# Optimization experiments

Measured on AMD Instinct MI355X. Metric: run time of the kernel, lower is better.

Reference implementation:

```python
import jax, jax.numpy as jnp
import numpy as np

EPS = 1e-3  # keras LayerNormalization default epsilon


def _layernorm(x, gamma, beta):
    mu = jnp.mean(x, axis=-1, keepdims=True)
    var = jnp.mean(jnp.square(x - mu), axis=-1, keepdims=True)
    return (x - mu) * jax.lax.rsqrt(var + EPS) * gamma + beta


def setup_inputs() -> dict:
    key = jax.random.key(0)
    B, T, D, H = 8, 2048, 192, 3
    KD = D           # TalkingHeadsAttention(key_dim=dim, value_dim=dim)
    HID = 4 * D      # mlp_ratio = 4.0
    ks = jax.random.split(key, 12)
    s_in = 0.02
    inp = {
        "x": jax.random.normal(ks[0], (B, T, D), jnp.float32),
        # norm1 / norm2
        "gamma1": jnp.ones((D,), jnp.float32),
        "beta1": jnp.zeros((D,), jnp.float32),
        "gamma2": jnp.ones((D,), jnp.float32),
        "beta2": jnp.zeros((D,), jnp.float32),
        # attention projections (qkv_bias=False -> no biases)
        "wq": jax.random.normal(ks[1], (D, H, KD), jnp.float32) * s_in,
        "wk": jax.random.normal(ks[2], (D, H, KD), jnp.float32) * s_in,
        "wv": jax.random.normal(ks[3], (D, H, KD), jnp.float32) * s_in,
        "wo": jax.random.normal(ks[4], (H, KD, D), jnp.float32) * s_in,
        # talking-heads mixing matrices [H, H]
        "pre_w": jnp.eye(H, dtype=jnp.float32) + jax.random.normal(ks[5], (H, H), jnp.float32) * 0.02,
        "post_w": jnp.eye(H, dtype=jnp.float32) + jax.random.normal(ks[6], (H, H), jnp.float32) * 0.02,
        # MLP (bias=True)
        "w1": jax.random.normal(ks[7], (D, HID), jnp.float32) * s_in,
        "b1": jnp.zeros((HID,), jnp.float32),
        "w2": jax.random.normal(ks[8], (HID, D), jnp.float32) * s_in,
        "b2": jnp.zeros((D,), jnp.float32),
    }
    return inp


def reference(x, gamma1, beta1, gamma2, beta2, wq, wk, wv, wo, pre_w, post_w, w1, b1, w2, b2):
    KD = wq.shape[-1]
    # --- pre-norm + talking-heads attention ---
    n = _layernorm(x, gamma1, beta1)                      # [B,T,D]
    q = jnp.einsum("btd,dhk->bthk", n, wq)               # [B,T,H,KD]
    k = jnp.einsum("bsd,dhk->bshk", n, wk)
    v = jnp.einsum("bsd,dhk->bshk", n, wv)
    scores = jnp.einsum("bthk,bshk->bhts", q, k) / jnp.sqrt(jnp.asarray(KD, x.dtype))
    scores = jnp.einsum("bhts,hg->bgts", scores, pre_w)   # pre-softmax head mix
    probs = jax.nn.softmax(scores, axis=-1)
    probs = jnp.einsum("bhts,hg->bgts", probs, post_w)    # post-softmax head mix
    ctx = jnp.einsum("bhts,bshk->bthk", probs, v)         # [B,T,H,KD]
    attn_out = jnp.einsum("bthk,hkd->btd", ctx, wo)       # [B,T,D]
    x = x + attn_out                                      # ls1/drop_path1 are Identity
    # --- pre-norm + MLP ---
    n2 = _layernorm(x, gamma2, beta2)
    h = jax.nn.gelu(n2 @ w1 + b1, approximate=False)      # keras gelu = exact erf
    mlp_out = h @ w2 + b2
    return x + mlp_out
```

## Files before the change

kernel.cpp:

```cpp
#include <hip/hip_runtime.h>
#include <hip/hip_bf16.h>

typedef __hip_bfloat16 bf16;
typedef unsigned char u8;
typedef __attribute__((ext_vector_type(8))) __bf16 bf16x8;
typedef __attribute__((ext_vector_type(4))) float f32x4;
typedef __attribute__((ext_vector_type(2))) float f32x2;

__device__ __forceinline__ void gld_lds16(const void* g, void* l) {
  __builtin_amdgcn_global_load_lds((const __attribute__((address_space(1))) void*)g,
                                   (__attribute__((address_space(3))) void*)l, 16, 0, 0);
}
__device__ __forceinline__ u8 f2e4m3(float v) {
  return (u8)(__builtin_amdgcn_cvt_pk_fp8_f32(v, 0.f, 0, false) & 0xff);
}
__device__ __forceinline__ f32x2 pk_mul(f32x2 a, f32x2 b) {
  f32x2 d;
  asm("v_pk_mul_f32 %0, %1, %2" : "=v"(d) : "v"(a), "v"(b));
  return d;
}
__device__ __forceinline__ f32x2 pk_fma(f32x2 a, f32x2 b, f32x2 c) {
  f32x2 d;
  asm("v_pk_fma_f32 %0, %1, %2, %3" : "=v"(d) : "v"(a), "v"(b), "v"(c));
  return d;
}

__global__ __launch_bounds__(256) void setup_k(
    const float* __restrict__ x, const float* __restrict__ gamma1, const float* __restrict__ beta1,
    const float* __restrict__ wq, const float* __restrict__ wk,
    const float* __restrict__ wv, const float* __restrict__ wo,
    const float* __restrict__ post_w, const float* __restrict__ w1, const float* __restrict__ w2,
    bf16* __restrict__ nb, bf16* __restrict__ WqkvT,
    bf16* __restrict__ w1T, bf16* __restrict__ w2f)
{
  const int bid = blockIdx.x;
  if (bid < 432) {
    const int j = bid * 256 + threadIdx.x;
    const int dd = j % 192;
    const int r = j / 192;
    const int h = r / 192, din = r % 192;
    float acc = 0.f;
    #pragma unroll
    for (int g2 = 0; g2 < 3; ++g2) {
      const float pw = post_w[h*3 + g2];
      const float* wvp = wv + (size_t)din*576 + g2*192;
      const float* wop = wo + (size_t)(g2*192)*192 + dd;
      float s0 = 0.f, s1 = 0.f, s2 = 0.f, s3 = 0.f;
      for (int kd = 0; kd < 192; kd += 4) {
        s0 += wvp[kd]     * wop[(size_t)kd*192];
        s1 += wvp[kd + 1] * wop[(size_t)(kd + 1)*192];
        s2 += wvp[kd + 2] * wop[(size_t)(kd + 2)*192];
        s3 += wvp[kd + 3] * wop[(size_t)(kd + 3)*192];
      }
      acc += pw * ((s0 + s1) + (s2 + s3));
    }
    WqkvT[(size_t)(1152 + h*192 + dd)*192 + din] = __float2bfloat16(acc);
    return;
  }
  if (bid < 2448) {
    int i = (bid - 432) * 256 + threadIdx.x;
    if (i < 221184) {
      int n = i / 192, d = i % 192;
      int sel = n / 576, c = n % 576, h = c / 192, kd = c % 192;
      const float* w = (sel == 0) ? wq : wk;
      WqkvT[i] = __float2bfloat16(w[(d*3 + h)*192 + kd]);
      return;
    }
    i -= 221184;
    if (i < 147456) {
      int j = i / 192, d = i % 192;
      w1T[i] = __float2bfloat16(w1[d*768 + j]);
      return;
    }
    i -= 147456;
    {
      int j = i / 192, d = i % 192;
      int c = j >> 6, ks = (j >> 5) & 1, l4 = (j >> 3) & 3, e = j & 7;
      int dn = d >> 4, l15 = d & 15;
      w2f[(size_t)((((c*2 + ks)*12 + dn)*64) + l4*16 + l15)*8 + e] =
          __float2bfloat16(w2[(size_t)j*192 + d]);
    }
    return;
  }
  {
    int row = (bid - 2448) * 4 + (threadIdx.x >> 6);
    int lane = threadIdx.x & 63;
    const float* xr = x + (size_t)row * 192;
    float v0 = xr[lane], v1 = xr[lane + 64], v2 = xr[lane + 128];
    float s = v0 + v1 + v2;
    #pragma unroll
    for (int o = 32; o; o >>= 1) s += __shfl_xor(s, o);
    float mu = s * (1.f / 192.f);
    float d0 = v0 - mu, d1 = v1 - mu, d2 = v2 - mu;
    float q = d0*d0 + d1*d1 + d2*d2;
    #pragma unroll
    for (int o = 32; o; o >>= 1) q += __shfl_xor(q, o);
    float rs = rsqrtf(q * (1.f / 192.f) + 1e-3f);
    bf16* orow = nb + (size_t)row * 192;
    orow[lane]       = __float2bfloat16(d0*rs*gamma1[lane]       + beta1[lane]);
    orow[lane + 64]  = __float2bfloat16(d1*rs*gamma1[lane + 64]  + beta1[lane + 64]);
    orow[lane + 128] = __float2bfloat16(d2*rs*gamma1[lane + 128] + beta1[lane + 128]);
  }
}

__global__ __launch_bounds__(256) void gemm_qkv(
    const bf16* __restrict__ A, const bf16* __restrict__ BT,
    u8* __restrict__ q_out, u8* __restrict__ k_out, u8* __restrict__ mt_out)
{
  const int K = 192;
  const int tid = threadIdx.x, lane = tid & 63, wid = tid >> 6;
  const int wm = wid >> 1, wn = wid & 1;
  const int row0 = blockIdx.y * 128, col0 = blockIdx.x * 64;
  __shared__ __align__(16) bf16 As[2][128 * 32];
  __shared__ __align__(16) bf16 Bs[2][64 * 32];
  f32x4 acc[4][2] = {};

#define STAGE(buf_, kt_) do { \
    const bf16* Ab_ = A + (size_t)row0 * K + (kt_) * 32; \
    int c0_ = tid, r0_ = c0_ >> 2, cc0_ = (c0_ & 3) << 3; \
    gld_lds16(Ab_ + (size_t)r0_ * K + cc0_, &As[buf_][c0_ * 8]); \
    int c1_ = tid + 256, r1_ = c1_ >> 2, cc1_ = (c1_ & 3) << 3; \
    gld_lds16(Ab_ + (size_t)r1_ * K + cc1_, &As[buf_][c1_ * 8]); \
    const bf16* Bb_ = BT + (size_t)col0 * K + (kt_) * 32; \
    gld_lds16(Bb_ + (size_t)(tid >> 2) * K + ((tid & 3) << 3), &Bs[buf_][tid * 8]); \
  } while (0)

  STAGE(0, 0);
  for (int kt = 0; kt < 6; ++kt) {
    __syncthreads();
    const int buf = kt & 1;
    if (kt + 1 < 6) STAGE(buf ^ 1, kt + 1);
    const int koff = (lane >> 4) * 8;
    bf16x8 af[4], bfr[2];
    #pragma unroll
    for (int m = 0; m < 4; ++m)
      af[m] = *(const bf16x8*)&As[buf][(wm*64 + m*16 + (lane & 15))*32 + koff];
    #pragma unroll
    for (int n = 0; n < 2; ++n)
      bfr[n] = *(const bf16x8*)&Bs[buf][(wn*32 + n*16 + (lane & 15))*32 + koff];
    #pragma unroll
    for (int m = 0; m < 4; ++m)
      #pragma unroll
      for (int n = 0; n < 2; ++n)
        acc[m][n] = __builtin_amdgcn_mfma_f32_16x16x32_bf16(af[m], bfr[n], acc[m][n], 0, 0, 0);
  }
#undef STAGE

  const int rbase = row0 + wm * 64;
  const int cbase = col0 + wn * 32;
  #pragma unroll
  for (int m = 0; m < 4; ++m) {
    #pragma unroll
    for (int n = 0; n < 2; ++n) {
      const int col = cbase + n*16 + (lane & 15);
      const int rtop = rbase + m*16 + ((lane >> 4) << 2);
      const int b = rtop >> 11, t_ = rtop & 2047;
      const int sel = col / 576, c2 = col % 576;
      const int h = c2 / 192, kd = c2 % 192;
      if (sel == 2) {
        int pk = __builtin_amdgcn_cvt_pk_fp8_f32(acc[m][n][0], acc[m][n][1], 0, false);
        pk = __builtin_amdgcn_cvt_pk_fp8_f32(acc[m][n][2], acc[m][n][3], pk, true);
        const size_t fo = ((((size_t)b*64 + (t_>>5))*3 + h)*12 + (kd>>4))*512
                        + (((kd&15) + (((t_>>3)&3)<<4))<<3) + (t_&4);
        *(unsigned*)&mt_out[fo] = (unsigned)pk;
      } else {
        #pragma unroll
        for (int j = 0; j < 4; ++j) {
          const int t = t_ + j;
          const size_t fo = ((((size_t)b*64 + (t>>5))*3 + h)*6 + (kd>>5))*1024
                          + (((t>>4)&1))*512
                          + (((t&15) + (((kd>>3)&3)<<4))<<3) + (kd&7);
          if (sel == 0) q_out[fo] = f2e4m3(acc[m][n][j]);
          else          k_out[fo] = f2e4m3(acc[m][n][j]);
        }
      }
    }
  }
}

__global__ __launch_bounds__(256, 2) void mlp_k(
    const bf16* __restrict__ nb, const bf16* __restrict__ w1T,
    const bf16* __restrict__ w2f, const float* __restrict__ b1,
    const float* __restrict__ b2, float* __restrict__ out)
{
  const int tid = threadIdx.x, lane = tid & 63, w = tid >> 6;
  const int l15 = lane & 15, l4 = lane >> 4;
  const int wm = w >> 1, wn = w & 1;
  const int row0 = blockIdx.x * 32;

  __shared__ __align__(16) bf16 As[6 * 32 * 32];
  __shared__ __align__(16) bf16 Bs[6 * 64 * 32];
  __shared__ __align__(16) bf16 Hs[32 * 72];

  #pragma unroll
  for (int i = 0; i < 3; ++i) {
    const int L = i * 256 + tid;
    const int kq = L >> 7, rem = L & 127, r = rem >> 2, sp = rem & 3;
    gld_lds16(nb + (size_t)(row0 + r) * 192 + kq*32 + sp*8, &As[L * 8]);
  }
#define STAGEB(c_) do { \
    _Pragma("unroll") \
    for (int i_ = 0; i_ < 6; ++i_) { \
      const int L_ = i_ * 256 + tid; \
      const int kq_ = L_ >> 8, rem_ = L_ & 255, r_ = rem_ >> 2, sp_ = rem_ & 3; \
      gld_lds16(w1T + (size_t)((c_)*64 + r_) * 192 + kq_*32 + sp_*8, &Bs[L_ * 8]); \
    } \
  } while (0)

  STAGEB(0);
  __syncthreads();

  f32x4 acc[2][3] = {};
  for (int c = 0; c < 12; ++c) {
    bf16x8 wf[3][2];
    #pragma unroll
    for (int n = 0; n < 3; ++n)
      #pragma unroll
      for (int ks = 0; ks < 2; ++ks)
        wf[n][ks] = *(const bf16x8*)(w2f + (size_t)((((c*2 + ks)*12) + w*3 + n)*64 + lane)*8);

    f32x4 sacc[2] = {};
    const int koff = l4*8;
    #pragma unroll
    for (int kq = 0; kq < 6; ++kq) {
      const bf16x8 af = *(const bf16x8*)&As[(kq*32 + wm*16 + l15)*32 + koff];
      #pragma unroll
      for (int n = 0; n < 2; ++n) {
        const bf16x8 bfr = *(const bf16x8*)&Bs[(kq*64 + wn*32 + n*16 + l15)*32 + koff];
        sacc[n] = __builtin_amdgcn_mfma_f32_16x16x32_bf16(af, bfr, sacc[n], 0, 0, 0);
      }
    }
    #pragma unroll
    for (int n = 0; n < 2; ++n) {
      const int jc = wn*32 + n*16 + l15;
      const float bv = b1[c*64 + jc];
      #pragma unroll
      for (int jr = 0; jr < 4; ++jr) {
        const float u = sacc[n][jr] + bv;
        const float g = 0.5f * u * (1.f + erff(u * 0.70710678118654752f));
        Hs[(wm*16 + l4*4 + jr)*72 + jc] = __float2bfloat16(g);
      }
    }
    __syncthreads();
    if (c + 1 < 12) STAGEB(c + 1);
    #pragma unroll
    for (int ks = 0; ks < 2; ++ks) {
      bf16x8 ha[2];
      #pragma unroll
      for (int m = 0; m < 2; ++m)
        ha[m] = *(const bf16x8*)&Hs[(m*16 + l15)*72 + ks*32 + l4*8];
      #pragma unroll
      for (int m = 0; m < 2; ++m)
        #pragma unroll
        for (int n = 0; n < 3; ++n)
          acc[m][n] = __builtin_amdgcn_mfma_f32_16x16x32_bf16(ha[m], wf[n][ks], acc[m][n], 0, 0, 0);
    }
    __syncthreads();
  }
#undef STAGEB

  #pragma unroll
  for (int n = 0; n < 3; ++n) {
    const int d = w*48 + n*16 + l15;
    const float b2v = b2[d];
    #pragma unroll
    for (int m = 0; m < 2; ++m) {
      #pragma unroll
      for (int jr = 0; jr < 4; ++jr) {
        const int t = m*16 + l4*4 + jr;
        const size_t idx = (size_t)(row0 + t)*192 + d;
        out[idx] = out[idx] + acc[m][n][jr] + b2v;
      }
    }
  }
}

__global__ __launch_bounds__(256, 2) void attn_k(
    const u8* __restrict__ q, const u8* __restrict__ kf,
    const u8* __restrict__ MT, const float* __restrict__ pre_w,
    const float* __restrict__ x, const float* __restrict__ gamma2,
    const float* __restrict__ beta2, float* __restrict__ out,
    bf16* __restrict__ nb)
{
  const int tid = threadIdx.x, lane = tid & 63, wv = tid >> 6;
  const int l15 = lane & 15, l4 = lane >> 4;
  const int tq = wv & 1, sq = wv >> 1;
  const int bid = blockIdx.x;
  const int b = bid & 7;
  const int tt = bid >> 3;
  const int t0 = tt * 32;

  __shared__ __align__(16) u8 Ks[2][18432];
  __shared__ __align__(16) u8 Ps[2][3072];
  __shared__ float rlPart[2][3][32];
  __shared__ float lnS[4][32][2];

  const u8* qfb = q + ((size_t)b*64 + tt) * 18432;
  long qf[3][6];
  #pragma unroll
  for (int h = 0; h < 3; ++h)
    #pragma unroll
    for (int kq = 0; kq < 6; ++kq)
      qf[h][kq] = *(const long*)(qfb + ((h*6 + kq)*2 + tq)*512 + lane*8);

  f32x2 pwf2[9];
  #pragma unroll
  for (int i = 0; i < 9; ++i) {
    const float v = pre_w[i] * 0.07216878364870323f * 1.44269504088896f;
    pwf2[i][0] = v; pwf2[i][1] = v;
  }

  f32x4 acc[3][2][3] = {};
  float sgacc[3] = {0.f, 0.f, 0.f};
  const int trow = tq*16 + l15;
  const int psw = (l15 >> 2) & 3;
  const int pwr = (((sq*2 + (l4 >> 1)) ^ psw) << 3) + ((l4 & 1) << 2);
  const int prd = (l4 ^ psw) << 3;

  const u8* kfb = kf + (size_t)b * 64 * 18432;
  const u8* mtb = MT + (size_t)b * 64 * 18432;

#define STAGEK(buf_, st_) do { \
    const u8* kb_ = kfb + (size_t)(st_) * 18432; \
    _Pragma("unroll") \
    for (int i_ = 0; i_ < 5; ++i_) { \
      const int L_ = i_ * 256 + tid; \
      if (L_ < 1152) gld_lds16(kb_ + L_*16, &Ks[buf_][L_*16]); \
    } \
  } while (0)

#define LOADMF(MF_, st_) do { \
    const u8* mb_ = mtb + (size_t)(st_) * 18432 + wv*3*512 + lane*8; \
    _Pragma("unroll") \
    for (int g_ = 0; g_ < 3; ++g_) \
      _Pragma("unroll") \
      for (int n_ = 0; n_ < 3; ++n_) \
        MF_[g_][n_] = *(const long*)(mb_ + (g_*12 + n_)*512); \
  } while (0)

#define PV(stm1_, MF_) do { \
    const int bp_ = (stm1_) & 1; \
    __builtin_amdgcn_s_setprio(1); \
    _Pragma("unroll") \
    for (int g_ = 0; g_ < 3; ++g_) \
      _Pragma("unroll") \
      for (int m_ = 0; m_ < 2; ++m_) { \
        const long pf_ = *(const long*)&Ps[bp_][g_*1024 + (m_*16 + l15)*32 + prd]; \
        _Pragma("unroll") \
        for (int n_ = 0; n_ < 3; ++n_) \
          acc[g_][m_][n_] = __builtin_amdgcn_mfma_f32_16x16x32_fp8_fp8(pf_, MF_[g_][n_], acc[g_][m_][n_], 0, 0, 0); \
      } \
    __builtin_amdgcn_s_setprio(0); \
  } while (0)

#define QKSM(st_) do { \
    const int bq_ = (st_) & 1; \
    f32x4 sacc0 = {}, sacc1 = {}, sacc2 = {}; \
    __builtin_amdgcn_s_setprio(1); \
    _Pragma("unroll") \
    for (int kq_ = 0; kq_ < 6; ++kq_) { \
      const long kf0_ = *(const long*)&Ks[bq_][((0*6 + kq_)*2 + sq)*512 + lane*8]; \
      sacc0 = __builtin_amdgcn_mfma_f32_16x16x32_fp8_fp8(kf0_, qf[0][kq_], sacc0, 0, 0, 0); \
      const long kf1_ = *(const long*)&Ks[bq_][((1*6 + kq_)*2 + sq)*512 + lane*8]; \
      sacc1 = __builtin_amdgcn_mfma_f32_16x16x32_fp8_fp8(kf1_, qf[1][kq_], sacc1, 0, 0, 0); \
      const long kf2_ = *(const long*)&Ks[bq_][((2*6 + kq_)*2 + sq)*512 + lane*8]; \
      sacc2 = __builtin_amdgcn_mfma_f32_16x16x32_fp8_fp8(kf2_, qf[2][kq_], sacc2, 0, 0, 0); \
    } \
    __builtin_amdgcn_s_setprio(0); \
    f32x2 p0a = {sacc0[0], sacc0[1]}, p0b = {sacc0[2], sacc0[3]}; \
    f32x2 p1a = {sacc1[0], sacc1[1]}, p1b = {sacc1[2], sacc1[3]}; \
    f32x2 p2a = {sacc2[0], sacc2[1]}, p2b = {sacc2[2], sacc2[3]}; \
    _Pragma("unroll") \
    for (int g_ = 0; g_ < 3; ++g_) { \
      f32x2 va = pk_mul(p0a, pwf2[g_]); \
      va = pk_fma(p1a, pwf2[3+g_], va); \
      va = pk_fma(p2a, pwf2[6+g_], va); \
      f32x2 vb = pk_mul(p0b, pwf2[g_]); \
      vb = pk_fma(p1b, pwf2[3+g_], vb); \
      vb = pk_fma(p2b, pwf2[6+g_], vb); \
      float e0_ = exp2f(va[0]), e1_ = exp2f(va[1]); \
      float e2_ = exp2f(vb[0]), e3_ = exp2f(vb[1]); \
      sgacc[g_] += (e0_ + e1_) + (e2_ + e3_); \
      int pk_ = __builtin_amdgcn_cvt_pk_fp8_f32(e0_, e1_, 0, false); \
      pk_ = __builtin_amdgcn_cvt_pk_fp8_f32(e2_, e3_, pk_, true); \
      *(unsigned*)&Ps[bq_][g_*1024 + trow*32 + pwr] = (unsigned)pk_; \
    } \
  } while (0)

  long mfA[3][3], mfB[3][3];

  STAGEK(0, 0);
  __syncthreads();
  STAGEK(1, 1);
  LOADMF(mfA, 0);
  QKSM(0);
  for (int st = 1; st < 63; st += 2) {
    __syncthreads();
    STAGEK((st + 1) & 1, st + 1);
    LOADMF(mfB, st);
    PV(st - 1, mfA);
    QKSM(st);
    __syncthreads();
    if (st + 2 < 64) STAGEK((st + 2) & 1, st + 2);
    LOADMF(mfA, st + 1);
    PV(st, mfB);
    QKSM(st + 1);
  }
  __syncthreads();
  LOADMF(mfB, 63);
  PV(62, mfA);
  QKSM(63);
  __syncthreads();
  PV(63, mfB);
  #pragma unroll
  for (int g = 0; g < 3; ++g) {
    float s = sgacc[g];
    s += __shfl_xor(s, 16);
    s += __shfl_xor(s, 32);
    if (l4 == 0) rlPart[sq][g][trow] = s;
  }
  __syncthreads();

  float ovv[2][3][4];
  #pragma unroll
  for (int m = 0; m < 2; ++m) {
    #pragma unroll
    for (int j = 0; j < 4; ++j) {
      const int row = m*16 + l4*4 + j;
      float rlv[3];
      #pragma unroll
      for (int g = 0; g < 3; ++g)
        rlv[g] = 1.f / (rlPart[0][g][row] + rlPart[1][g][row]);
      float s = 0.f, ss = 0.f;
      #pragma unroll
      for (int n = 0; n < 3; ++n) {
        const int d = wv*48 + n*16 + l15;
        const size_t idx = ((size_t)b*2048 + t0 + row)*192 + d;
        const float ov = x[idx] + rlv[0]*acc[0][m][n][j] + rlv[1]*acc[1][m][n][j]
                                + rlv[2]*acc[2][m][n][j];
        out[idx] = ov;
        ovv[m][n][j] = ov;
        s += ov; ss += ov*ov;
      }
      #pragma unroll
      for (int o = 1; o < 16; o <<= 1) { s += __shfl_xor(s, o); ss += __shfl_xor(ss, o); }
      if (l15 == 0) { lnS[wv][row][0] = s; lnS[wv][row][1] = ss; }
    }
  }
  __syncthreads();

  float gmL[3], btL[3];
  #pragma unroll
  for (int n = 0; n < 3; ++n) {
    const int d = wv*48 + n*16 + l15;
    gmL[n] = gamma2[d]; btL[n] = beta2[d];
  }
  #pragma unroll
  for (int m = 0; m < 2; ++m) {
    #pragma unroll
    for (int j = 0; j < 4; ++j) {
      const int row = m*16 + l4*4 + j;
      const float ts  = lnS[0][row][0] + lnS[1][row][0] + lnS[2][row][0] + lnS[3][row][0];
      const float tss = lnS[0][row][1] + lnS[1][row][1] + lnS[2][row][1] + lnS[3][row][1];
      const float mu = ts * (1.f / 192.f);
      const float rs = rsqrtf(tss * (1.f / 192.f) - mu*mu + 1e-3f);
      #pragma unroll
      for (int n = 0; n < 3; ++n) {
        const int d = wv*48 + n*16 + l15;
        nb[((size_t)b*2048 + t0 + row)*192 + d] =
            __float2bfloat16((ovv[m][n][j] - mu) * rs * gmL[n] + btL[n]);
      }
    }
  }
#undef STAGEK
#undef LOADMF
#undef PV
#undef QKSM
}

extern "C" void kernel_launch(void* const* d_in, const int* in_sizes, int n_in,
                              void* d_out, int out_size, void* d_ws, size_t ws_size,
                              hipStream_t stream)
{
  (void)in_sizes; (void)n_in; (void)out_size; (void)ws_size;
  const float* x      = (const float*)d_in[0];
  const float* gamma1 = (const float*)d_in[1];
  const float* beta1  = (const float*)d_in[2];
  const float* gamma2 = (const float*)d_in[3];
  const float* beta2  = (const float*)d_in[4];
  const float* wq     = (const float*)d_in[5];
  const float* wk     = (const float*)d_in[6];
  const float* wv     = (const float*)d_in[7];
  const float* wo     = (const float*)d_in[8];
  const float* pre_w  = (const float*)d_in[9];
  const float* post_w = (const float*)d_in[10];
  const float* w1     = (const float*)d_in[11];
  const float* b1     = (const float*)d_in[12];
  const float* w2     = (const float*)d_in[13];
  const float* b2     = (const float*)d_in[14];
  float* out = (float*)d_out;

  uint8_t* base = (uint8_t*)d_ws;
  size_t off = 0;
  auto alloc = [&](size_t bytes) {
    uint8_t* r = base + off; off += (bytes + 255) & ~(size_t)255; return r;
  };
  bf16* nb      = (bf16*)alloc((size_t)16384 * 192 * 2);
  u8*   qb      = (u8*)alloc((size_t)9437184);
  u8*   kb      = (u8*)alloc((size_t)9437184);
  u8*   MTslab  = (u8*)alloc((size_t)9437184);
  bf16* WqkvT   = (bf16*)alloc((size_t)331776 * 2);
  bf16* w1T     = (bf16*)alloc((size_t)147456 * 2);
  bf16* w2f     = (bf16*)alloc((size_t)147456 * 2);

  setup_k<<<6544, 256, 0, stream>>>(x, gamma1, beta1, wq, wk, wv, wo, post_w, w1, w2,
                                    nb, WqkvT, w1T, w2f);
  gemm_qkv<<<dim3(27, 128, 1), 256, 0, stream>>>(nb, WqkvT, qb, kb, MTslab);
  attn_k<<<512, 256, 0, stream>>>(qb, kb, MTslab, pre_w, x, gamma2, beta2, out, nb);
  mlp_k<<<512, 256, 0, stream>>>(nb, w1T, w2f, b1, b2, out);
}
```

Measured before the change: 172.3 us.

## Fuse MLP into attention kernel epilogue, reusing shared memory

```diff
diff --git a/kernel.cpp b/kernel.cpp
--- a/kernel.cpp
+++ b/kernel.cpp
@@ -178,109 +178,13 @@
   }
 }
 
-__global__ __launch_bounds__(256, 2) void mlp_k(
-    const bf16* __restrict__ nb, const bf16* __restrict__ w1T,
-    const bf16* __restrict__ w2f, const float* __restrict__ b1,
-    const float* __restrict__ b2, float* __restrict__ out)
-{
-  const int tid = threadIdx.x, lane = tid & 63, w = tid >> 6;
-  const int l15 = lane & 15, l4 = lane >> 4;
-  const int wm = w >> 1, wn = w & 1;
-  const int row0 = blockIdx.x * 32;
-
-  __shared__ __align__(16) bf16 As[6 * 32 * 32];
-  __shared__ __align__(16) bf16 Bs[6 * 64 * 32];
-  __shared__ __align__(16) bf16 Hs[32 * 72];
-
-  #pragma unroll
-  for (int i = 0; i < 3; ++i) {
-    const int L = i * 256 + tid;
-    const int kq = L >> 7, rem = L & 127, r = rem >> 2, sp = rem & 3;
-    gld_lds16(nb + (size_t)(row0 + r) * 192 + kq*32 + sp*8, &As[L * 8]);
-  }
-#define STAGEB(c_) do { \
-    _Pragma("unroll") \
-    for (int i_ = 0; i_ < 6; ++i_) { \
-      const int L_ = i_ * 256 + tid; \
-      const int kq_ = L_ >> 8, rem_ = L_ & 255, r_ = rem_ >> 2, sp_ = rem_ & 3; \
-      gld_lds16(w1T + (size_t)((c_)*64 + r_) * 192 + kq_*32 + sp_*8, &Bs[L_ * 8]); \
-    } \
-  } while (0)
-
-  STAGEB(0);
-  __syncthreads();
-
-  f32x4 acc[2][3] = {};
-  for (int c = 0; c < 12; ++c) {
-    bf16x8 wf[3][2];
-    #pragma unroll
-    for (int n = 0; n < 3; ++n)
-      #pragma unroll
-      for (int ks = 0; ks < 2; ++ks)
-        wf[n][ks] = *(const bf16x8*)(w2f + (size_t)((((c*2 + ks)*12) + w*3 + n)*64 + lane)*8);
-
-    f32x4 sacc[2] = {};
-    const int koff = l4*8;
-    #pragma unroll
-    for (int kq = 0; kq < 6; ++kq) {
-      const bf16x8 af = *(const bf16x8*)&As[(kq*32 + wm*16 + l15)*32 + koff];
-      #pragma unroll
-      for (int n = 0; n < 2; ++n) {
-        const bf16x8 bfr = *(const bf16x8*)&Bs[(kq*64 + wn*32 + n*16 + l15)*32 + koff];
-        sacc[n] = __builtin_amdgcn_mfma_f32_16x16x32_bf16(af, bfr, sacc[n], 0, 0, 0);
-      }
-    }
-    #pragma unroll
-    for (int n = 0; n < 2; ++n) {
-      const int jc = wn*32 + n*16 + l15;
-      const float bv = b1[c*64 + jc];
-      #pragma unroll
-      for (int jr = 0; jr < 4; ++jr) {
-        const float u = sacc[n][jr] + bv;
-        const float g = 0.5f * u * (1.f + erff(u * 0.70710678118654752f));
-        Hs[(wm*16 + l4*4 + jr)*72 + jc] = __float2bfloat16(g);
-      }
-    }
-    __syncthreads();
-    if (c + 1 < 12) STAGEB(c + 1);
-    #pragma unroll
-    for (int ks = 0; ks < 2; ++ks) {
-      bf16x8 ha[2];
-      #pragma unroll
-      for (int m = 0; m < 2; ++m)
-        ha[m] = *(const bf16x8*)&Hs[(m*16 + l15)*72 + ks*32 + l4*8];
-      #pragma unroll
-      for (int m = 0; m < 2; ++m)
-        #pragma unroll
-        for (int n = 0; n < 3; ++n)
-          acc[m][n] = __builtin_amdgcn_mfma_f32_16x16x32_bf16(ha[m], wf[n][ks], acc[m][n], 0, 0, 0);
-    }
-    __syncthreads();
-  }
-#undef STAGEB
-
-  #pragma unroll
-  for (int n = 0; n < 3; ++n) {
-    const int d = w*48 + n*16 + l15;
-    const float b2v = b2[d];
-    #pragma unroll
-    for (int m = 0; m < 2; ++m) {
-      #pragma unroll
-      for (int jr = 0; jr < 4; ++jr) {
-        const int t = m*16 + l4*4 + jr;
-        const size_t idx = (size_t)(row0 + t)*192 + d;
-        out[idx] = out[idx] + acc[m][n][jr] + b2v;
-      }
-    }
-  }
-}
-
 __global__ __launch_bounds__(256, 2) void attn_k(
     const u8* __restrict__ q, const u8* __restrict__ kf,
     const u8* __restrict__ MT, const float* __restrict__ pre_w,
     const float* __restrict__ x, const float* __restrict__ gamma2,
-    const float* __restrict__ beta2, float* __restrict__ out,
-    bf16* __restrict__ nb)
+    const float* __restrict__ beta2, const bf16* __restrict__ w1T,
+    const bf16* __restrict__ w2f, const float* __restrict__ b1,
+    const float* __restrict__ b2, float* __restrict__ out)
 {
   const int tid = threadIdx.x, lane = tid & 63, wv = tid >> 6;
   const int l15 = lane & 15, l4 = lane >> 4;
@@ -290,10 +194,14 @@
   const int tt = bid >> 3;
   const int t0 = tt * 32;
 
-  __shared__ __align__(16) u8 Ks[2][18432];
-  __shared__ __align__(16) u8 Ps[2][3072];
+  __shared__ __align__(16) u8 S[43008];
   __shared__ float rlPart[2][3][32];
   __shared__ float lnS[4][32][2];
+  u8* KsP = S;
+  u8* PsP = S + 36864;
+  bf16* N2 = (bf16*)S;
+  bf16* BsP = (bf16*)(S + 12800);
+  bf16* HsP = (bf16*)(S + 37376);
 
   const u8* qfb = q + ((size_t)b*64 + tt) * 18432;
   long qf[3][6];
@@ -325,7 +233,7 @@
     _Pragma("unroll") \
     for (int i_ = 0; i_ < 5; ++i_) { \
       const int L_ = i_ * 256 + tid; \
-      if (L_ < 1152) gld_lds16(kb_ + L_*16, &Ks[buf_][L_*16]); \
+      if (L_ < 1152) gld_lds16(kb_ + L_*16, KsP + (buf_)*18432 + L_*16); \
     } \
   } while (0)
 
@@ -345,7 +253,7 @@
     for (int g_ = 0; g_ < 3; ++g_) \
       _Pragma("unroll") \
       for (int m_ = 0; m_ < 2; ++m_) { \
-        const long pf_ = *(const long*)&Ps[bp_][g_*1024 + (m_*16 + l15)*32 + prd]; \
+        const long pf_ = *(const long*)(PsP + bp_*3072 + g_*1024 + (m_*16 + l15)*32 + prd); \
         _Pragma("unroll") \
         for (int n_ = 0; n_ < 3; ++n_) \
           acc[g_][m_][n_] = __builtin_amdgcn_mfma_f32_16x16x32_fp8_fp8(pf_, MF_[g_][n_], acc[g_][m_][n_], 0, 0, 0); \
@@ -359,11 +267,11 @@
     __builtin_amdgcn_s_setprio(1); \
     _Pragma("unroll") \
     for (int kq_ = 0; kq_ < 6; ++kq_) { \
-      const long kf0_ = *(const long*)&Ks[bq_][((0*6 + kq_)*2 + sq)*512 + lane*8]; \
+      const long kf0_ = *(const long*)(KsP + bq_*18432 + (((0*6 + kq_)*2 + sq)*512) + lane*8); \
       sacc0 = __builtin_amdgcn_mfma_f32_16x16x32_fp8_fp8(kf0_, qf[0][kq_], sacc0, 0, 0, 0); \
-      const long kf1_ = *(const long*)&Ks[bq_][((1*6 + kq_)*2 + sq)*512 + lane*8]; \
+      const long kf1_ = *(const long*)(KsP + bq_*18432 + (((1*6 + kq_)*2 + sq)*512) + lane*8); \
       sacc1 = __builtin_amdgcn_mfma_f32_16x16x32_fp8_fp8(kf1_, qf[1][kq_], sacc1, 0, 0, 0); \
-      const long kf2_ = *(const long*)&Ks[bq_][((2*6 + kq_)*2 + sq)*512 + lane*8]; \
+      const long kf2_ = *(const long*)(KsP + bq_*18432 + (((2*6 + kq_)*2 + sq)*512) + lane*8); \
       sacc2 = __builtin_amdgcn_mfma_f32_16x16x32_fp8_fp8(kf2_, qf[2][kq_], sacc2, 0, 0, 0); \
     } \
     __builtin_amdgcn_s_setprio(0); \
@@ -383,7 +291,16 @@
       sgacc[g_] += (e0_ + e1_) + (e2_ + e3_); \
       int pk_ = __builtin_amdgcn_cvt_pk_fp8_f32(e0_, e1_, 0, false); \
       pk_ = __builtin_amdgcn_cvt_pk_fp8_f32(e2_, e3_, pk_, true); \
-      *(unsigned*)&Ps[bq_][g_*1024 + trow*32 + pwr] = (unsigned)pk_; \
+      *(unsigned*)(PsP + bq_*3072 + g_*1024 + trow*32 + pwr) = (unsigned)pk_; \
+    } \
+  } while (0)
+
+#define STAGEB(c_) do { \
+    _Pragma("unroll") \
+    for (int i_ = 0; i_ < 6; ++i_) { \
+      const int L_ = i_ * 256 + tid; \
+      const int kq_ = L_ >> 8, rem_ = L_ & 255, r_ = rem_ >> 2, sp_ = rem_ & 3; \
+      gld_lds16(w1T + (size_t)((c_)*64 + r_) * 192 + kq_*32 + sp_*8, (u8*)BsP + L_*16); \
     } \
   } while (0)
 
@@ -412,6 +329,7 @@
   QKSM(63);
   __syncthreads();
   PV(63, mfB);
+  STAGEB(0);
   #pragma unroll
   for (int g = 0; g < 3; ++g) {
     float s = sgacc[g];
@@ -438,7 +356,6 @@
         const size_t idx = ((size_t)b*2048 + t0 + row)*192 + d;
         const float ov = x[idx] + rlv[0]*acc[0][m][n][j] + rlv[1]*acc[1][m][n][j]
                                 + rlv[2]*acc[2][m][n][j];
-        out[idx] = ov;
         ovv[m][n][j] = ov;
         s += ov; ss += ov*ov;
       }
@@ -449,26 +366,91 @@
   }
   __syncthreads();
 
-  float gmL[3], btL[3];
+  {
+    float gmL[3], btL[3];
+    #pragma unroll
+    for (int n = 0; n < 3; ++n) {
+      const int d = wv*48 + n*16 + l15;
+      gmL[n] = gamma2[d]; btL[n] = beta2[d];
+    }
+    #pragma unroll
+    for (int m = 0; m < 2; ++m) {
+      #pragma unroll
+      for (int j = 0; j < 4; ++j) {
+        const int row = m*16 + l4*4 + j;
+        const float ts  = lnS[0][row][0] + lnS[1][row][0] + lnS[2][row][0] + lnS[3][row][0];
+        const float tss = lnS[0][row][1] + lnS[1][row][1] + lnS[2][row][1] + lnS[3][row][1];
+        const float mu = ts * (1.f / 192.f);
+        const float rs = rsqrtf(tss * (1.f / 192.f) - mu*mu + 1e-3f);
+        #pragma unroll
+        for (int n = 0; n < 3; ++n) {
+          const int d = wv*48 + n*16 + l15;
+          N2[row*200 + d] = __float2bfloat16((ovv[m][n][j] - mu) * rs * gmL[n] + btL[n]);
+        }
+      }
+    }
+  }
+  __syncthreads();
+
+  const int wm = wv >> 1, wn = wv & 1;
+  f32x4 macc[2][3] = {};
+  for (int c = 0; c < 12; ++c) {
+    bf16x8 wf[3][2];
+    #pragma unroll
+    for (int n = 0; n < 3; ++n)
+      #pragma unroll
+      for (int ks = 0; ks < 2; ++ks)
+        wf[n][ks] = *(const bf16x8*)(w2f + (size_t)((((c*2 + ks)*12) + wv*3 + n)*64 + lane)*8);
+
+    f32x4 sacc[2] = {};
+    #pragma unroll
+    for (int kq = 0; kq < 6; ++kq) {
+      const bf16x8 af = *(const bf16x8*)&N2[(wm*16 + l15)*200 + kq*32 + l4*8];
+      #pragma unroll
+      for (int n = 0; n < 2; ++n) {
+        const bf16x8 bfr = *(const bf16x8*)&BsP[(kq*64 + wn*32 + n*16 + l15)*32 + l4*8];
+        sacc[n] = __builtin_amdgcn_mfma_f32_16x16x32_bf16(af, bfr, sacc[n], 0, 0, 0);
+      }
+    }
+    #pragma unroll
+    for (int n = 0; n < 2; ++n) {
+      const int jc = wn*32 + n*16 + l15;
+      const float bv = b1[c*64 + jc];
+      #pragma unroll
+      for (int jr = 0; jr < 4; ++jr) {
+        const float u = sacc[n][jr] + bv;
+        const float g = 0.5f * u * (1.f + erff(u * 0.70710678118654752f));
+        HsP[(wm*16 + l4*4 + jr)*72 + jc] = __float2bfloat16(g);
+      }
+    }
+    __syncthreads();
+    if (c + 1 < 12) STAGEB(c + 1);
+    #pragma unroll
+    for (int ks = 0; ks < 2; ++ks) {
+      bf16x8 ha[2];
+      #pragma unroll
+      for (int m = 0; m < 2; ++m)
+        ha[m] = *(const bf16x8*)&HsP[(m*16 + l15)*72 + ks*32 + l4*8];
+      #pragma unroll
+      for (int m = 0; m < 2; ++m)
+        #pragma unroll
+        for (int n = 0; n < 3; ++n)
+          macc[m][n] = __builtin_amdgcn_mfma_f32_16x16x32_bf16(ha[m], wf[n][ks], macc[m][n], 0, 0, 0);
+    }
+    __syncthreads();
+  }
+
   #pragma unroll
   for (int n = 0; n < 3; ++n) {
     const int d = wv*48 + n*16 + l15;
-    gmL[n] = gamma2[d]; btL[n] = beta2[d];
-  }
-  #pragma unroll
-  for (int m = 0; m < 2; ++m) {
-    #pragma unroll
-    for (int j = 0; j < 4; ++j) {
-      const int row = m*16 + l4*4 + j;
-      const float ts  = lnS[0][row][0] + lnS[1][row][0] + lnS[2][row][0] + lnS[3][row][0];
-      const float tss = lnS[0][row][1] + lnS[1][row][1] + lnS[2][row][1] + lnS[3][row][1];
-      const float mu = ts * (1.f / 192.f);
-      const float rs = rsqrtf(tss * (1.f / 192.f) - mu*mu + 1e-3f);
-      #pragma unroll
-      for (int n = 0; n < 3; ++n) {
-        const int d = wv*48 + n*16 + l15;
-        nb[((size_t)b*2048 + t0 + row)*192 + d] =
-            __float2bfloat16((ovv[m][n][j] - mu) * rs * gmL[n] + btL[n]);
+    const float b2v = b2[d];
+    #pragma unroll
+    for (int m = 0; m < 2; ++m) {
+      #pragma unroll
+      for (int jr = 0; jr < 4; ++jr) {
+        const int row = m*16 + l4*4 + jr;
+        const size_t idx = ((size_t)b*2048 + t0 + row)*192 + d;
+        out[idx] = ovv[m][n][jr] + macc[m][n][jr] + b2v;
       }
     }
   }
@@ -476,6 +458,7 @@
 #undef LOADMF
 #undef PV
 #undef QKSM
+#undef STAGEB
 }
 
 extern "C" void kernel_launch(void* const* d_in, const int* in_sizes, int n_in,
@@ -516,6 +499,6 @@
   setup_k<<<6544, 256, 0, stream>>>(x, gamma1, beta1, wq, wk, wv, wo, post_w, w1, w2,
                                     nb, WqkvT, w1T, w2f);
   gemm_qkv<<<dim3(27, 128, 1), 256, 0, stream>>>(nb, WqkvT, qb, kb, MTslab);
-  attn_k<<<512, 256, 0, stream>>>(qb, kb, MTslab, pre_w, x, gamma2, beta2, out, nb);
-  mlp_k<<<512, 256, 0, stream>>>(nb, w1T, w2f, b1, b2, out);
-}
+  attn_k<<<512, 256, 0, stream>>>(qb, kb, MTslab, pre_w, x, gamma2, beta2,
+                                  w1T, w2f, b1, b2, out);
+}
```

Measured after the change: 168.1 us. -2.4%, faster.
